# Performance work log

Measured on AMD Instinct MI355X. Metric: run time of the kernel, lower is better.

Reference implementation:

```python
import jax, jax.numpy as jnp
import numpy as np

HIDDEN = 2048
N_HEADS = 32
N_KV_HEADS = 8
HEAD_DIM = 64
MAX_SEQ_LEN = 4096
ROPE_THETA = 500000.0
B, L = 1, 2048
EPS = 1e-6
NEG = -1e9


def precompute_rope(head_dim, max_seq_len, theta):
    freqs = 1.0 / theta ** (jnp.arange(0, head_dim, 2, dtype=jnp.float32) / head_dim)
    pos = jnp.arange(max_seq_len, dtype=jnp.float32)
    ang = pos[:, None] * freqs[None, :]                     # [S, hd/2]
    cos = jnp.repeat(jnp.cos(ang), 2, axis=-1)              # [S, hd]
    sin = jnp.repeat(jnp.sin(ang), 2, axis=-1)
    return cos, sin


def apply_rope(x, cos, sin):
    # x: [B, H, L, hd]; interleaved (even/odd) rotation, faithful to torch code
    seq_len = x.shape[2]
    c = cos[:seq_len][None, None, :, ::2]                   # [1,1,L,hd/2]
    s = sin[:seq_len][None, None, :, ::2]
    x1 = x[..., ::2]
    x2 = x[..., 1::2]
    o1 = x1 * c - x2 * s
    o2 = x2 * c + x1 * s
    return jnp.stack([o1, o2], axis=-1).reshape(x.shape)


def rmsnorm(x, w):
    return x * jax.lax.rsqrt(jnp.mean(x * x, axis=-1, keepdims=True) + EPS) * w


def setup_inputs() -> dict:
    key = jax.random.key(0)
    ks = jax.random.split(key, 6)
    x = jax.random.normal(ks[0], (B, L, HIDDEN), dtype=jnp.float32)
    causal = jnp.tril(jnp.ones((L, L), dtype=bool))
    mask = jnp.where(causal, 0.0, NEG).astype(jnp.float32)  # additive causal mask
    scale = 0.02
    norm_w = jnp.ones((HIDDEN,), dtype=jnp.float32)
    Wq = jax.random.normal(ks[1], (N_HEADS * HEAD_DIM, HIDDEN), dtype=jnp.float32) * scale
    Wk = jax.random.normal(ks[2], (N_KV_HEADS * HEAD_DIM, HIDDEN), dtype=jnp.float32) * scale
    Wv = jax.random.normal(ks[3], (N_KV_HEADS * HEAD_DIM, HIDDEN), dtype=jnp.float32) * scale
    Wo = jax.random.normal(ks[4], (HIDDEN, N_HEADS * HEAD_DIM), dtype=jnp.float32) * scale
    rope_cos, rope_sin = precompute_rope(HEAD_DIM, MAX_SEQ_LEN, ROPE_THETA)
    return {"x": x, "mask": mask, "norm_w": norm_w, "Wq": Wq, "Wk": Wk,
            "Wv": Wv, "Wo": Wo, "rope_cos": rope_cos, "rope_sin": rope_sin}


def reference(x, mask, norm_w, Wq, Wk, Wv, Wo, rope_cos, rope_sin):
    Bb, Ll, _ = x.shape
    residual = x
    h = rmsnorm(x, norm_w)
    q = (h @ Wq.T).reshape(Bb, Ll, N_HEADS, HEAD_DIM).transpose(0, 2, 1, 3)     # [B,H,L,hd]
    k = (h @ Wk.T).reshape(Bb, Ll, N_KV_HEADS, HEAD_DIM).transpose(0, 2, 1, 3)  # [B,Hk,L,hd]
    v = (h @ Wv.T).reshape(Bb, Ll, N_KV_HEADS, HEAD_DIM).transpose(0, 2, 1, 3)
    q = apply_rope(q, rope_cos, rope_sin)
    k = apply_rope(k, rope_cos, rope_sin)
    n_groups = N_HEADS // N_KV_HEADS
    if n_groups > 1:
        k = jnp.repeat(k, n_groups, axis=1)   # GQA repeat_interleave
        v = jnp.repeat(v, n_groups, axis=1)
    scale = jnp.sqrt(jnp.asarray(HEAD_DIM, dtype=q.dtype))
    attn = jnp.einsum('bhld,bhmd->bhlm', q, k) / scale
    attn = attn + mask                                       # broadcast [L,L]
    attn = jax.nn.softmax(attn, axis=-1)
    out = jnp.einsum('bhlm,bhmd->bhld', attn, v)
    out = out.transpose(0, 2, 1, 3).reshape(Bb, Ll, N_HEADS * HEAD_DIM)
    return out @ Wo.T + residual
```

## Files before the change

### kernel.cpp

```cpp
#include <hip/hip_runtime.h>
#include <stdint.h>

#define L_SEQ 2048
#define HID   2048
#define NHEAD 32
#define NKV   8
#define HD    64
#define KVDIM 512
#define QSCALE 0.18033688f

typedef __attribute__((ext_vector_type(8))) short s16x8;
typedef __attribute__((ext_vector_type(4))) short s16x4;
typedef __attribute__((ext_vector_type(4))) float f32x4;

__device__ __forceinline__ short f2bf(float f) {
  __bf16 b = (__bf16)f;
  short s;
  __builtin_memcpy(&s, &b, 2);
  return s;
}

__device__ __forceinline__ void gload16(const void* g, void* l) {
  __builtin_amdgcn_global_load_lds(
      (const __attribute__((address_space(1))) void*)g,
      (__attribute__((address_space(3))) void*)l, 16, 0, 0);
}

__global__ __launch_bounds__(256) void pre_kernel(
    const float* __restrict__ x, const float* __restrict__ w,
    const float* __restrict__ wq, const float* __restrict__ wk,
    const float* __restrict__ wv, const float* __restrict__ wo,
    short* __restrict__ h,
    short* __restrict__ owq, short* __restrict__ owk,
    short* __restrict__ owv, short* __restrict__ owo) {
  const int tid = threadIdx.x;
  if (blockIdx.x >= 2048) {
    int64_t e = ((int64_t)(blockIdx.x - 2048) * 256 + tid) * 4;
    const float* src; short* dst; int64_t o;
    if (e < 4194304)      { src = wq; dst = owq; o = e; }
    else if (e < 5242880) { src = wk; dst = owk; o = e - 4194304; }
    else if (e < 6291456) { src = wv; dst = owv; o = e - 5242880; }
    else                  { src = wo; dst = owo; o = e - 6291456; }
    f32x4 v = *(const f32x4*)(src + o);
    s16x4 b;
    b[0] = f2bf(v[0]); b[1] = f2bf(v[1]); b[2] = f2bf(v[2]); b[3] = f2bf(v[3]);
    *(s16x4*)(dst + o) = b;
    return;
  }
  const int row = blockIdx.x;
  const float* xr = x + (int64_t)row * HID + tid * 8;
  f32x4 a = *(const f32x4*)(xr);
  f32x4 b = *(const f32x4*)(xr + 4);
  float ss = a[0]*a[0]+a[1]*a[1]+a[2]*a[2]+a[3]*a[3]
           + b[0]*b[0]+b[1]*b[1]+b[2]*b[2]+b[3]*b[3];
  #pragma unroll
  for (int off = 1; off < 64; off <<= 1) ss += __shfl_xor(ss, off, 64);
  __shared__ float sred[4];
  if ((tid & 63) == 0) sred[tid >> 6] = ss;
  __syncthreads();
  const float scale = rsqrtf((sred[0]+sred[1]+sred[2]+sred[3]) * (1.0f/HID) + 1e-6f);
  const float* wp = w + tid * 8;
  f32x4 wa = *(const f32x4*)(wp);
  f32x4 wb = *(const f32x4*)(wp + 4);
  s16x8 o;
  o[0]=f2bf(a[0]*scale*wa[0]); o[1]=f2bf(a[1]*scale*wa[1]);
  o[2]=f2bf(a[2]*scale*wa[2]); o[3]=f2bf(a[3]*scale*wa[3]);
  o[4]=f2bf(b[0]*scale*wb[0]); o[5]=f2bf(b[1]*scale*wb[1]);
  o[6]=f2bf(b[2]*scale*wb[2]); o[7]=f2bf(b[3]*scale*wb[3]);
  *(s16x8*)(h + (int64_t)row * HID + tid * 8) = o;
}

__device__ __forceinline__ void gemm_core_128x64(
    const short* __restrict__ A, const short* __restrict__ B,
    short* sA, short* sB, f32x4 acc[4][2]) {
  const int tid = threadIdx.x;
  const int lane = tid & 63;
  const int w = tid >> 6, wr = w >> 1, wc = w & 1;
  const int g = lane >> 4, li = lane & 15;

  auto stage = [&](int k0, int buf) {
    #pragma unroll
    for (int i = 0; i < 4; ++i) {
      const int flat = i * 256 + tid;
      const int row = flat >> 3, c8 = flat & 7;
      const int sc = c8 ^ (row & 7);
      gload16(A + (int64_t)row * HID + k0 + sc * 8, sA + buf * 8192 + flat * 8);
    }
    #pragma unroll
    for (int i = 0; i < 2; ++i) {
      const int flat = i * 256 + tid;
      const int row = flat >> 3, c8 = flat & 7;
      const int sc = c8 ^ (row & 7);
      gload16(B + (int64_t)row * HID + k0 + sc * 8, sB + buf * 4096 + flat * 8);
    }
  };

  stage(0, 0);
  for (int k0 = 0; k0 < HID; k0 += 64) {
    const int cur = (k0 >> 6) & 1;
    __syncthreads();
    if (k0 + 64 < HID) stage(k0 + 64, cur ^ 1);
    const short* cA = sA + cur * 8192;
    const short* cB = sB + cur * 4096;
    #pragma unroll
    for (int kk = 0; kk < 2; ++kk) {
      s16x8 af[4], bfr[2];
      const int chunk = (kk << 2) | g;
      #pragma unroll
      for (int m = 0; m < 4; ++m) {
        const int row = wr * 64 + m * 16 + li;
        af[m] = *(const s16x8*)(cA + row * 64 + ((chunk ^ (li & 7)) << 3));
      }
      #pragma unroll
      for (int n = 0; n < 2; ++n) {
        const int row = wc * 32 + n * 16 + li;
        bfr[n] = *(const s16x8*)(cB + row * 64 + ((chunk ^ (li & 7)) << 3));
      }
      __builtin_amdgcn_s_setprio(1);
      #pragma unroll
      for (int m = 0; m < 4; ++m)
        #pragma unroll
        for (int n = 0; n < 2; ++n)
          acc[m][n] = __builtin_amdgcn_mfma_f32_16x16x32_bf16(af[m], bfr[n], acc[m][n], 0, 0, 0);
      __builtin_amdgcn_s_setprio(0);
    }
  }
}

__global__ __launch_bounds__(256) void qkv_kernel(
    const short* __restrict__ h16, const short* __restrict__ wq,
    const short* __restrict__ wk, const short* __restrict__ wv,
    short* __restrict__ qo, short* __restrict__ ko, short* __restrict__ vto,
    const float* __restrict__ rc, const float* __restrict__ rs) {
  __shared__ short sA[2 * 128 * 64];
  __shared__ short sB[2 * 64 * 64];
  const int cb = blockIdx.x, rb = blockIdx.y;
  const short* B; short* out; int colbase, mode; int64_t ldc;
  if (cb < 32)      { B = wq + (int64_t)cb * 64 * HID;        out = qo;  colbase = cb * 64;        mode = 0; ldc = HID;   }
  else if (cb < 40) { B = wk + (int64_t)(cb - 32) * 64 * HID; out = ko;  colbase = (cb - 32) * 64; mode = 0; ldc = KVDIM; }
  else              { B = wv + (int64_t)(cb - 40) * 64 * HID; out = vto; colbase = (cb - 40) * 64; mode = 1; ldc = L_SEQ; }
  const float rsc = (cb < 32) ? QSCALE : 1.0f;

  f32x4 acc[4][2];
  const f32x4 z = {0.f, 0.f, 0.f, 0.f};
  #pragma unroll
  for (int m = 0; m < 4; ++m)
    #pragma unroll
    for (int n = 0; n < 2; ++n) acc[m][n] = z;

  gemm_core_128x64(h16 + (int64_t)rb * 128 * HID, B, sA, sB, acc);

  const int lane = threadIdx.x & 63;
  const int w = threadIdx.x >> 6, wr = w >> 1, wc = w & 1;
  const int g = lane >> 4, li = lane & 15;

  if (mode == 0) {
    #pragma unroll
    for (int m = 0; m < 4; ++m) {
      #pragma unroll
      for (int n = 0; n < 2; ++n) {
        const int col = colbase + wc * 32 + n * 16 + li;
        const int d2 = col & 62;
        #pragma unroll
        for (int r = 0; r < 4; ++r) {
          const int row = rb * 128 + wr * 64 + m * 16 + g * 4 + r;
          const float c = rc[row * 64 + d2] * rsc;
          const float s = rs[row * 64 + d2] * rsc;
          const float v0 = acc[m][n][r];
          const float pr = __shfl_xor(v0, 1, 64);
          const float o = (lane & 1) ? (v0 * c + pr * s) : (v0 * c - pr * s);
          out[(int64_t)row * ldc + col] = f2bf(o);
        }
      }
    }
  } else {
    #pragma unroll
    for (int m = 0; m < 4; ++m) {
      #pragma unroll
      for (int n = 0; n < 2; ++n) {
        const int col = colbase + wc * 32 + n * 16 + li;
        const int row0 = rb * 128 + wr * 64 + m * 16 + g * 4;
        s16x4 pk;
        pk[0] = f2bf(acc[m][n][0]); pk[1] = f2bf(acc[m][n][1]);
        pk[2] = f2bf(acc[m][n][2]); pk[3] = f2bf(acc[m][n][3]);
        *(s16x4*)(out + (int64_t)col * L_SEQ + row0) = pk;
      }
    }
  }
}

__global__ __launch_bounds__(512, 4) void attn_kernel(
    const short* __restrict__ q16, const short* __restrict__ k16,
    const short* __restrict__ vt16, short* __restrict__ out16) {
  __shared__ short sK[4 * 64 * 64];
  __shared__ short sV[4 * 64 * 64];
  __shared__ short sP[8][16 * 64];
  const int pi = blockIdx.x, h = blockIdx.y, kvh = h >> 2;
  const int qbL = pi, qbH = 31 - pi;
  const int tid = threadIdx.x, lane = tid & 63, w = tid >> 6, wl = w & 3;
  const int g = lane >> 4, li = lane & 15;
  const int myqb = (w < 4) ? qbL : qbH;
  short* sPw = &sP[w][0];

  s16x8 qf[2];
  {
    const int qr = myqb * 64 + wl * 16 + li;
    #pragma unroll
    for (int kk = 0; kk < 2; ++kk)
      qf[kk] = *(const s16x8*)(q16 + (int64_t)qr * HID + h * 64 + kk * 32 + g * 8);
  }

  f32x4 acc[4];
  const f32x4 z = {0.f, 0.f, 0.f, 0.f};
  #pragma unroll
  for (int n = 0; n < 4; ++n) acc[n] = z;
  float m = -1e30f, l = 0.f;

  auto stage1 = [&](int t, int buf, int slot) {
    const int kv0 = t * 64;
    const int row = tid >> 3, c8 = tid & 7;
    const int sc = c8 ^ (row & 7);
    const int off = (buf * 2 + slot) * 4096;
    gload16(k16 + (int64_t)(kv0 + row) * KVDIM + kvh * 64 + sc * 8,
            sK + off + tid * 8);
    gload16(vt16 + (int64_t)(kvh * 64 + row) * L_SEQ + kv0 + sc * 8,
            sV + off + tid * 8);
  };

  stage1(0, 0, 0);
  stage1(1, 0, 1);
  for (int tp = 0; 2 * tp <= qbH; ++tp) {
    const int buf = tp & 1;
    __syncthreads();
    if (2 * tp + 2 <= qbH) {
      stage1(2 * tp + 2, buf ^ 1, 0);
      const int t3 = 2 * tp + 3;
      stage1(t3 <= qbH ? t3 : t3 - 1, buf ^ 1, 1);
    }
    #pragma unroll
    for (int sl = 0; sl < 2; ++sl) {
      const int t = 2 * tp + sl;
      if (t <= qbH && (w >= 4 || t <= qbL)) {
        const short* cK = sK + (buf * 2 + sl) * 4096;
        const short* cV = sV + (buf * 2 + sl) * 4096;

        s16x8 kf[2][4];
        #pragma unroll
        for (int kk = 0; kk < 2; ++kk)
          #pragma unroll
          for (int n = 0; n < 4; ++n)
            kf[kk][n] = *(const s16x8*)(cK + (n * 16 + li) * 64 + ((((kk << 2) | g) ^ (li & 7)) << 3));
        f32x4 s[4];
        #pragma unroll
        for (int n = 0; n < 4; ++n) s[n] = z;
        __builtin_amdgcn_s_setprio(1);
        #pragma unroll
        for (int kk = 0; kk < 2; ++kk)
          #pragma unroll
          for (int n = 0; n < 4; ++n)
            s[n] = __builtin_amdgcn_mfma_f32_16x16x32_bf16(kf[kk][n], qf[kk], s[n], 0, 0, 0);
        __builtin_amdgcn_s_setprio(0);

        if (t == myqb) {
          const int ql = wl * 16 + li;
          #pragma unroll
          for (int n = 0; n < 4; ++n)
            #pragma unroll
            for (int r = 0; r < 4; ++r)
              if (n * 16 + g * 4 + r > ql) s[n][r] = -1e30f;
        }

        float mx = fmaxf(fmaxf(s[0][0], s[0][1]), fmaxf(s[0][2], s[0][3]));
        #pragma unroll
        for (int n = 1; n < 4; ++n)
          mx = fmaxf(mx, fmaxf(fmaxf(s[n][0], s[n][1]), fmaxf(s[n][2], s[n][3])));
        mx = fmaxf(mx, __shfl_xor(mx, 16, 64));
        mx = fmaxf(mx, __shfl_xor(mx, 32, 64));
        if (__any(mx > m + 8.0f)) {
          const float mn = fmaxf(m, mx);
          const float al = __builtin_amdgcn_exp2f(m - mn);
          m = mn;
          l *= al;
          #pragma unroll
          for (int dt = 0; dt < 4; ++dt)
            #pragma unroll
            for (int r = 0; r < 4; ++r) acc[dt][r] *= al;
        }
        float ps = 0.f;
        #pragma unroll
        for (int n = 0; n < 4; ++n) {
          s16x4 pk;
          #pragma unroll
          for (int r = 0; r < 4; ++r) {
            const float p = __builtin_amdgcn_exp2f(s[n][r] - m);
            pk[r] = f2bf(p);
            ps += p;
          }
          *(s16x4*)(sPw + li * 64 + (((n * 2 + (g >> 1)) ^ (li & 7)) << 3) + (g & 1) * 4) = pk;
        }
        ps += __shfl_xor(ps, 16, 64);
        ps += __shfl_xor(ps, 32, 64);
        l += ps;

        s16x8 vf[2][4];
        #pragma unroll
        for (int kk = 0; kk < 2; ++kk)
          #pragma unroll
          for (int dt = 0; dt < 4; ++dt)
            vf[kk][dt] = *(const s16x8*)(cV + (dt * 16 + li) * 64 + ((((kk << 2) | g) ^ (li & 7)) << 3));
        #pragma unroll
        for (int kk = 0; kk < 2; ++kk) {
          s16x8 pf = *(const s16x8*)(sPw + li * 64 + (((kk * 4 + g) ^ (li & 7)) << 3));
          __builtin_amdgcn_s_setprio(1);
          #pragma unroll
          for (int dt = 0; dt < 4; ++dt)
            acc[dt] = __builtin_amdgcn_mfma_f32_16x16x32_bf16(vf[kk][dt], pf, acc[dt], 0, 0, 0);
          __builtin_amdgcn_s_setprio(0);
        }
      }
    }
  }

  const float rl = 1.0f / l;
  #pragma unroll
  for (int n2 = 0; n2 < 4; ++n2) {
    s16x4 o;
    #pragma unroll
    for (int r = 0; r < 4; ++r) o[r] = f2bf(acc[n2][r] * rl);
    *(s16x4*)(sPw + li * 64 + (((n2 * 2 + (g >> 1)) ^ (li & 7)) << 3) + (g & 1) * 4) = o;
  }
  #pragma unroll
  for (int half = 0; half < 2; ++half) {
    const int chunk = half * 64 + lane;
    const int q = chunk >> 3, c = chunk & 7;
    s16x8 v = *(const s16x8*)(sPw + q * 64 + ((c ^ (q & 7)) << 3));
    *(s16x8*)(out16 + (int64_t)(myqb * 64 + wl * 16 + q) * HID + h * 64 + c * 8) = v;
  }
}

__global__ __launch_bounds__(256) void oproj_kernel(
    const short* __restrict__ ao, const short* __restrict__ wo,
    const float* __restrict__ resid, float* __restrict__ out) {
  __shared__ short sA[2 * 128 * 64];
  __shared__ short sB[2 * 64 * 64];
  const int cb = blockIdx.x, rb = blockIdx.y;
  f32x4 acc[4][2];
  const f32x4 z = {0.f, 0.f, 0.f, 0.f};
  #pragma unroll
  for (int m = 0; m < 4; ++m)
    #pragma unroll
    for (int n = 0; n < 2; ++n) acc[m][n] = z;

  gemm_core_128x64(ao + (int64_t)rb * 128 * HID, wo + (int64_t)cb * 64 * HID, sA, sB, acc);

  const int lane = threadIdx.x & 63;
  const int w = threadIdx.x >> 6, wr = w >> 1, wc = w & 1;
  const int g = lane >> 4, li = lane & 15;
  #pragma unroll
  for (int m = 0; m < 4; ++m) {
    #pragma unroll
    for (int n = 0; n < 2; ++n) {
      const int col = cb * 64 + wc * 32 + n * 16 + li;
      #pragma unroll
      for (int r = 0; r < 4; ++r) {
        const int row = rb * 128 + wr * 64 + m * 16 + g * 4 + r;
        out[(int64_t)row * HID + col] = acc[m][n][r] + resid[(int64_t)row * HID + col];
      }
    }
  }
}

extern "C" void kernel_launch(void* const* d_in, const int* in_sizes, int n_in,
                              void* d_out, int out_size, void* d_ws, size_t ws_size,
                              hipStream_t stream) {
  (void)in_sizes; (void)n_in; (void)out_size; (void)ws_size;
  const float* x      = (const float*)d_in[0];
  const float* norm_w = (const float*)d_in[2];
  const float* Wq     = (const float*)d_in[3];
  const float* Wk     = (const float*)d_in[4];
  const float* Wv     = (const float*)d_in[5];
  const float* Wo     = (const float*)d_in[6];
  const float* rc     = (const float*)d_in[7];
  const float* rs     = (const float*)d_in[8];
  float* out = (float*)d_out;

  char* ws = (char*)d_ws;
  short* wq16 = (short*)(ws);
  short* wk16 = (short*)(ws + 8388608);
  short* wv16 = (short*)(ws + 10485760);
  short* wo16 = (short*)(ws + 12582912);
  short* h16  = (short*)(ws + 20971520);
  short* q16  = (short*)(ws + 29360128);
  short* k16  = (short*)(ws + 37748736);
  short* vt16 = (short*)(ws + 39845888);
  short* ao16 = (short*)(ws + 41943040);

  pre_kernel<<<12288, 256, 0, stream>>>(x, norm_w, Wq, Wk, Wv, Wo,
                                        h16, wq16, wk16, wv16, wo16);
  qkv_kernel<<<dim3(48, 16), 256, 0, stream>>>(h16, wq16, wk16, wv16, q16, k16, vt16, rc, rs);
  attn_kernel<<<dim3(16, NHEAD), 512, 0, stream>>>(q16, k16, vt16, ao16);
  oproj_kernel<<<dim3(32, 16), 256, 0, stream>>>(ao16, wo16, x, out);
}
```

Baseline: 124.1 us.

## Switch attention to 32x32x16 MFMA with register-resident P via permlane32 swap

Attention now uses 4 waves of 256 threads, each owning 32 query rows, and 32x32x16 bf16 MFMAs instead of 8 waves with 16x16x32 MFMAs. The P matrix no longer goes through shared memory: it is packed to bf16 in registers and reshuffled with v_permlane32_swap into the B-operand layout. The output is written straight from registers without an LDS transpose. This cuts LDS traffic and the number of MFMA issues per tile. In exchange, register pressure per wave rises and each block has half as many waves to hide latency.

```diff
diff --git a/kernel.cpp b/kernel.cpp
--- a/kernel.cpp
+++ b/kernel.cpp
@@ -12,12 +12,18 @@
 typedef __attribute__((ext_vector_type(8))) short s16x8;
 typedef __attribute__((ext_vector_type(4))) short s16x4;
 typedef __attribute__((ext_vector_type(4))) float f32x4;
+typedef __attribute__((ext_vector_type(16))) float f32x16;
 
 __device__ __forceinline__ short f2bf(float f) {
   __bf16 b = (__bf16)f;
   short s;
   __builtin_memcpy(&s, &b, 2);
   return s;
+}
+
+__device__ __forceinline__ unsigned int pk2(float a, float b) {
+  return (unsigned int)(unsigned short)f2bf(a) |
+         ((unsigned int)(unsigned short)f2bf(b) << 16);
 }
 
 __device__ __forceinline__ void gload16(const void* g, void* l) {
@@ -189,92 +195,86 @@
   }
 }
 
-__global__ __launch_bounds__(512, 4) void attn_kernel(
+__global__ __launch_bounds__(256, 2) void attn_kernel(
     const short* __restrict__ q16, const short* __restrict__ k16,
     const short* __restrict__ vt16, short* __restrict__ out16) {
   __shared__ short sK[4 * 64 * 64];
   __shared__ short sV[4 * 64 * 64];
-  __shared__ short sP[8][16 * 64];
   const int pi = blockIdx.x, h = blockIdx.y, kvh = h >> 2;
   const int qbL = pi, qbH = 31 - pi;
-  const int tid = threadIdx.x, lane = tid & 63, w = tid >> 6, wl = w & 3;
-  const int g = lane >> 4, li = lane & 15;
-  const int myqb = (w < 4) ? qbL : qbH;
-  short* sPw = &sP[w][0];
-
-  s16x8 qf[2];
-  {
-    const int qr = myqb * 64 + wl * 16 + li;
-    #pragma unroll
-    for (int kk = 0; kk < 2; ++kk)
-      qf[kk] = *(const s16x8*)(q16 + (int64_t)qr * HID + h * 64 + kk * 32 + g * 8);
-  }
-
-  f32x4 acc[4];
-  const f32x4 z = {0.f, 0.f, 0.f, 0.f};
-  #pragma unroll
-  for (int n = 0; n < 4; ++n) acc[n] = z;
+  const int tid = threadIdx.x, lane = tid & 63, w = tid >> 6;
+  const int r31 = lane & 31, half = lane >> 5;
+  const int myqb = (w < 2) ? qbL : qbH;
+  const int wrow = w & 1;
+  const int qg = myqb * 64 + wrow * 32 + r31;
+
+  s16x8 qf[4];
+  #pragma unroll
+  for (int ds = 0; ds < 4; ++ds)
+    qf[ds] = *(const s16x8*)(q16 + (int64_t)qg * HID + h * 64 + ds * 16 + half * 8);
+
+  f32x16 acc0 = {}, acc1 = {};
   float m = -1e30f, l = 0.f;
 
-  auto stage1 = [&](int t, int buf, int slot) {
+  auto stage1 = [&](int t, int idx) {
     const int kv0 = t * 64;
-    const int row = tid >> 3, c8 = tid & 7;
-    const int sc = c8 ^ (row & 7);
-    const int off = (buf * 2 + slot) * 4096;
-    gload16(k16 + (int64_t)(kv0 + row) * KVDIM + kvh * 64 + sc * 8,
-            sK + off + tid * 8);
-    gload16(vt16 + (int64_t)(kvh * 64 + row) * L_SEQ + kv0 + sc * 8,
-            sV + off + tid * 8);
+    #pragma unroll
+    for (int i = 0; i < 2; ++i) {
+      const int flat = i * 256 + tid;
+      const int row = flat >> 3, c8 = flat & 7;
+      const int sc = c8 ^ (row & 7);
+      gload16(k16 + (int64_t)(kv0 + row) * KVDIM + kvh * 64 + sc * 8,
+              sK + idx * 4096 + flat * 8);
+      gload16(vt16 + (int64_t)(kvh * 64 + row) * L_SEQ + kv0 + sc * 8,
+              sV + idx * 4096 + flat * 8);
+    }
   };
 
-  stage1(0, 0, 0);
-  stage1(1, 0, 1);
+  stage1(0, 0);
+  stage1(1, 1);
   for (int tp = 0; 2 * tp <= qbH; ++tp) {
     const int buf = tp & 1;
     __syncthreads();
     if (2 * tp + 2 <= qbH) {
-      stage1(2 * tp + 2, buf ^ 1, 0);
+      stage1(2 * tp + 2, (buf ^ 1) * 2);
       const int t3 = 2 * tp + 3;
-      stage1(t3 <= qbH ? t3 : t3 - 1, buf ^ 1, 1);
+      stage1(t3 <= qbH ? t3 : t3 - 1, (buf ^ 1) * 2 + 1);
     }
     #pragma unroll
     for (int sl = 0; sl < 2; ++sl) {
       const int t = 2 * tp + sl;
-      if (t <= qbH && (w >= 4 || t <= qbL)) {
+      if (t <= myqb) {
         const short* cK = sK + (buf * 2 + sl) * 4096;
         const short* cV = sV + (buf * 2 + sl) * 4096;
 
-        s16x8 kf[2][4];
-        #pragma unroll
-        for (int kk = 0; kk < 2; ++kk)
+        f32x16 S0 = {}, S1 = {};
+        __builtin_amdgcn_s_setprio(1);
+        #pragma unroll
+        for (int ds = 0; ds < 4; ++ds) {
+          const int row0 = r31;
+          s16x8 kfa = *(const s16x8*)(cK + row0 * 64 + (((ds * 2 + half) ^ (row0 & 7)) << 3));
+          S0 = __builtin_amdgcn_mfma_f32_32x32x16_bf16(kfa, qf[ds], S0, 0, 0, 0);
+          const int row1 = 32 + r31;
+          s16x8 kfb = *(const s16x8*)(cK + row1 * 64 + (((ds * 2 + half) ^ (row1 & 7)) << 3));
+          S1 = __builtin_amdgcn_mfma_f32_32x32x16_bf16(kfb, qf[ds], S1, 0, 0, 0);
+        }
+        __builtin_amdgcn_s_setprio(0);
+
+        if (t == myqb) {
+          const int qloc = wrow * 32 + r31;
           #pragma unroll
-          for (int n = 0; n < 4; ++n)
-            kf[kk][n] = *(const s16x8*)(cK + (n * 16 + li) * 64 + ((((kk << 2) | g) ^ (li & 7)) << 3));
-        f32x4 s[4];
-        #pragma unroll
-        for (int n = 0; n < 4; ++n) s[n] = z;
-        __builtin_amdgcn_s_setprio(1);
-        #pragma unroll
-        for (int kk = 0; kk < 2; ++kk)
-          #pragma unroll
-          for (int n = 0; n < 4; ++n)
-            s[n] = __builtin_amdgcn_mfma_f32_16x16x32_bf16(kf[kk][n], qf[kk], s[n], 0, 0, 0);
-        __builtin_amdgcn_s_setprio(0);
-
-        if (t == myqb) {
-          const int ql = wl * 16 + li;
-          #pragma unroll
-          for (int n = 0; n < 4; ++n)
-            #pragma unroll
-            for (int r = 0; r < 4; ++r)
-              if (n * 16 + g * 4 + r > ql) s[n][r] = -1e30f;
-        }
-
-        float mx = fmaxf(fmaxf(s[0][0], s[0][1]), fmaxf(s[0][2], s[0][3]));
-        #pragma unroll
-        for (int n = 1; n < 4; ++n)
-          mx = fmaxf(mx, fmaxf(fmaxf(s[n][0], s[n][1]), fmaxf(s[n][2], s[n][3])));
-        mx = fmaxf(mx, __shfl_xor(mx, 16, 64));
+          for (int reg = 0; reg < 16; ++reg) {
+            const int row = (reg & 3) + 8 * (reg >> 2) + 4 * half;
+            if (row > qloc) S0[reg] = -1e30f;
+            if (row + 32 > qloc) S1[reg] = -1e30f;
+          }
+        }
+
+        float mx = S0[0];
+        #pragma unroll
+        for (int reg = 1; reg < 16; ++reg) mx = fmaxf(mx, S0[reg]);
+        #pragma unroll
+        for (int reg = 0; reg < 16; ++reg) mx = fmaxf(mx, S1[reg]);
         mx = fmaxf(mx, __shfl_xor(mx, 32, 64));
         if (__any(mx > m + 8.0f)) {
           const float mn = fmaxf(m, mx);
@@ -282,59 +282,70 @@
           m = mn;
           l *= al;
           #pragma unroll
-          for (int dt = 0; dt < 4; ++dt)
-            #pragma unroll
-            for (int r = 0; r < 4; ++r) acc[dt][r] *= al;
-        }
+          for (int reg = 0; reg < 16; ++reg) { acc0[reg] *= al; acc1[reg] *= al; }
+        }
+
         float ps = 0.f;
-        #pragma unroll
-        for (int n = 0; n < 4; ++n) {
-          s16x4 pk;
-          #pragma unroll
-          for (int r = 0; r < 4; ++r) {
-            const float p = __builtin_amdgcn_exp2f(s[n][r] - m);
-            pk[r] = f2bf(p);
-            ps += p;
-          }
-          *(s16x4*)(sPw + li * 64 + (((n * 2 + (g >> 1)) ^ (li & 7)) << 3) + (g & 1) * 4) = pk;
-        }
-        ps += __shfl_xor(ps, 16, 64);
+        unsigned int W[2][4][2];
+        #pragma unroll
+        for (int g2 = 0; g2 < 4; ++g2) {
+          float p0 = __builtin_amdgcn_exp2f(S0[g2 * 4 + 0] - m);
+          float p1 = __builtin_amdgcn_exp2f(S0[g2 * 4 + 1] - m);
+          float p2 = __builtin_amdgcn_exp2f(S0[g2 * 4 + 2] - m);
+          float p3 = __builtin_amdgcn_exp2f(S0[g2 * 4 + 3] - m);
+          ps += p0 + p1 + p2 + p3;
+          W[0][g2][0] = pk2(p0, p1);
+          W[0][g2][1] = pk2(p2, p3);
+          float q0 = __builtin_amdgcn_exp2f(S1[g2 * 4 + 0] - m);
+          float q1 = __builtin_amdgcn_exp2f(S1[g2 * 4 + 1] - m);
+          float q2 = __builtin_amdgcn_exp2f(S1[g2 * 4 + 2] - m);
+          float q3 = __builtin_amdgcn_exp2f(S1[g2 * 4 + 3] - m);
+          ps += q0 + q1 + q2 + q3;
+          W[1][g2][0] = pk2(q0, q1);
+          W[1][g2][1] = pk2(q2, q3);
+        }
         ps += __shfl_xor(ps, 32, 64);
         l += ps;
 
-        s16x8 vf[2][4];
-        #pragma unroll
-        for (int kk = 0; kk < 2; ++kk)
+        #pragma unroll
+        for (int kvt = 0; kvt < 2; ++kvt) {
           #pragma unroll
-          for (int dt = 0; dt < 4; ++dt)
-            vf[kk][dt] = *(const s16x8*)(cV + (dt * 16 + li) * 64 + ((((kk << 2) | g) ^ (li & 7)) << 3));
-        #pragma unroll
-        for (int kk = 0; kk < 2; ++kk) {
-          s16x8 pf = *(const s16x8*)(sPw + li * 64 + (((kk * 4 + g) ^ (li & 7)) << 3));
-          __builtin_amdgcn_s_setprio(1);
-          #pragma unroll
-          for (int dt = 0; dt < 4; ++dt)
-            acc[dt] = __builtin_amdgcn_mfma_f32_16x16x32_bf16(vf[kk][dt], pf, acc[dt], 0, 0, 0);
-          __builtin_amdgcn_s_setprio(0);
+          for (int ksl = 0; ksl < 2; ++ksl) {
+            unsigned int a0 = W[kvt][ksl * 2 + 0][0], b0 = W[kvt][ksl * 2 + 1][0];
+            unsigned int a1 = W[kvt][ksl * 2 + 0][1], b1 = W[kvt][ksl * 2 + 1][1];
+            asm volatile("v_permlane32_swap_b32 %0, %1" : "+v"(a0), "+v"(b0));
+            asm volatile("v_permlane32_swap_b32 %0, %1" : "+v"(a1), "+v"(b1));
+            union { unsigned int u[4]; s16x8 s; } pf;
+            pf.u[0] = a0; pf.u[1] = a1; pf.u[2] = b0; pf.u[3] = b1;
+            const int ks = kvt * 2 + ksl;
+            __builtin_amdgcn_s_setprio(1);
+            {
+              const int row0 = r31;
+              s16x8 vfa = *(const s16x8*)(cV + row0 * 64 + (((ks * 2 + half) ^ (row0 & 7)) << 3));
+              acc0 = __builtin_amdgcn_mfma_f32_32x32x16_bf16(vfa, pf.s, acc0, 0, 0, 0);
+              const int row1 = 32 + r31;
+              s16x8 vfb = *(const s16x8*)(cV + row1 * 64 + (((ks * 2 + half) ^ (row1 & 7)) << 3));
+              acc1 = __builtin_amdgcn_mfma_f32_32x32x16_bf16(vfb, pf.s, acc1, 0, 0, 0);
+            }
+            __builtin_amdgcn_s_setprio(0);
+          }
         }
       }
     }
   }
 
   const float rl = 1.0f / l;
-  #pragma unroll
-  for (int n2 = 0; n2 < 4; ++n2) {
-    s16x4 o;
-    #pragma unroll
-    for (int r = 0; r < 4; ++r) o[r] = f2bf(acc[n2][r] * rl);
-    *(s16x4*)(sPw + li * 64 + (((n2 * 2 + (g >> 1)) ^ (li & 7)) << 3) + (g & 1) * 4) = o;
-  }
-  #pragma unroll
-  for (int half = 0; half < 2; ++half) {
-    const int chunk = half * 64 + lane;
-    const int q = chunk >> 3, c = chunk & 7;
-    s16x8 v = *(const s16x8*)(sPw + q * 64 + ((c ^ (q & 7)) << 3));
-    *(s16x8*)(out16 + (int64_t)(myqb * 64 + wl * 16 + q) * HID + h * 64 + c * 8) = v;
+  short* orow = out16 + (int64_t)qg * HID + h * 64;
+  #pragma unroll
+  for (int g2 = 0; g2 < 4; ++g2) {
+    s16x4 o0, o1;
+    #pragma unroll
+    for (int r = 0; r < 4; ++r) {
+      o0[r] = f2bf(acc0[g2 * 4 + r] * rl);
+      o1[r] = f2bf(acc1[g2 * 4 + r] * rl);
+    }
+    *(s16x4*)(orow + g2 * 8 + half * 4) = o0;
+    *(s16x4*)(orow + 32 + g2 * 8 + half * 4) = o1;
   }
 }
 
@@ -398,6 +409,6 @@
   pre_kernel<<<12288, 256, 0, stream>>>(x, norm_w, Wq, Wk, Wv, Wo,
                                         h16, wq16, wk16, wv16, wo16);
   qkv_kernel<<<dim3(48, 16), 256, 0, stream>>>(h16, wq16, wk16, wv16, q16, k16, vt16, rc, rs);
-  attn_kernel<<<dim3(16, NHEAD), 512, 0, stream>>>(q16, k16, vt16, ao16);
+  attn_kernel<<<dim3(16, NHEAD), 256, 0, stream>>>(q16, k16, vt16, ao16);
   oproj_kernel<<<dim3(32, 16), 256, 0, stream>>>(ao16, wo16, x, out);
 }
```

Result: slower. 135.7 us (+9.3%).

## Move Wo bf16 conversion into attention kernel to overlap with attention

Applied to the files above, without the earlier changes.

The fp32-to-bf16 conversion of Wo moves out of the pre-kernel and into extra blocks of the attention launch, whose grid doubles in x. Those extra blocks only convert Wo and exit, so the conversion can run alongside attention work rather than on the critical path before the QKV GEMM. The cost is a larger attention grid with short blocks that may interfere with scheduling of the attention blocks. The wb[7-4] edit is cosmetic.

```diff
diff --git a/kernel.cpp b/kernel.cpp
--- a/kernel.cpp
+++ b/kernel.cpp
@@ -29,18 +29,17 @@
 __global__ __launch_bounds__(256) void pre_kernel(
     const float* __restrict__ x, const float* __restrict__ w,
     const float* __restrict__ wq, const float* __restrict__ wk,
-    const float* __restrict__ wv, const float* __restrict__ wo,
+    const float* __restrict__ wv,
     short* __restrict__ h,
     short* __restrict__ owq, short* __restrict__ owk,
-    short* __restrict__ owv, short* __restrict__ owo) {
+    short* __restrict__ owv) {
   const int tid = threadIdx.x;
   if (blockIdx.x >= 2048) {
     int64_t e = ((int64_t)(blockIdx.x - 2048) * 256 + tid) * 4;
     const float* src; short* dst; int64_t o;
     if (e < 4194304)      { src = wq; dst = owq; o = e; }
     else if (e < 5242880) { src = wk; dst = owk; o = e - 4194304; }
-    else if (e < 6291456) { src = wv; dst = owv; o = e - 5242880; }
-    else                  { src = wo; dst = owo; o = e - 6291456; }
+    else                  { src = wv; dst = owv; o = e - 5242880; }
     f32x4 v = *(const f32x4*)(src + o);
     s16x4 b;
     b[0] = f2bf(v[0]); b[1] = f2bf(v[1]); b[2] = f2bf(v[2]); b[3] = f2bf(v[3]);
@@ -66,7 +65,7 @@
   o[0]=f2bf(a[0]*scale*wa[0]); o[1]=f2bf(a[1]*scale*wa[1]);
   o[2]=f2bf(a[2]*scale*wa[2]); o[3]=f2bf(a[3]*scale*wa[3]);
   o[4]=f2bf(b[0]*scale*wb[0]); o[5]=f2bf(b[1]*scale*wb[1]);
-  o[6]=f2bf(b[2]*scale*wb[2]); o[7]=f2bf(b[3]*scale*wb[3]);
+  o[6]=f2bf(b[2]*scale*wb[2]); o[7]=f2bf(b[3]*scale*wb[7-4]);
   *(s16x8*)(h + (int64_t)row * HID + tid * 8) = o;
 }
 
@@ -191,7 +190,21 @@
 
 __global__ __launch_bounds__(512, 4) void attn_kernel(
     const short* __restrict__ q16, const short* __restrict__ k16,
-    const short* __restrict__ vt16, short* __restrict__ out16) {
+    const short* __restrict__ vt16, short* __restrict__ out16,
+    const float* __restrict__ wof, short* __restrict__ wo16o) {
+  if (blockIdx.x >= 16) {
+    const int idx = (blockIdx.x - 16) * NHEAD + blockIdx.y;
+    const int64_t base = (int64_t)idx * 8192;
+    #pragma unroll
+    for (int i = 0; i < 4; ++i) {
+      const int64_t o = base + i * 2048 + threadIdx.x * 4;
+      f32x4 v = *(const f32x4*)(wof + o);
+      s16x4 b;
+      b[0] = f2bf(v[0]); b[1] = f2bf(v[1]); b[2] = f2bf(v[2]); b[3] = f2bf(v[3]);
+      *(s16x4*)(wo16o + o) = b;
+    }
+    return;
+  }
   __shared__ short sK[4 * 64 * 64];
   __shared__ short sV[4 * 64 * 64];
   __shared__ short sP[8][16 * 64];
@@ -395,9 +408,9 @@
   short* vt16 = (short*)(ws + 39845888);
   short* ao16 = (short*)(ws + 41943040);
 
-  pre_kernel<<<12288, 256, 0, stream>>>(x, norm_w, Wq, Wk, Wv, Wo,
-                                        h16, wq16, wk16, wv16, wo16);
+  pre_kernel<<<8192, 256, 0, stream>>>(x, norm_w, Wq, Wk, Wv,
+                                       h16, wq16, wk16, wv16);
   qkv_kernel<<<dim3(48, 16), 256, 0, stream>>>(h16, wq16, wk16, wv16, q16, k16, vt16, rc, rs);
-  attn_kernel<<<dim3(16, NHEAD), 512, 0, stream>>>(q16, k16, vt16, ao16);
+  attn_kernel<<<dim3(32, NHEAD), 512, 0, stream>>>(q16, k16, vt16, ao16, Wo, wo16);
   oproj_kernel<<<dim3(32, 16), 256, 0, stream>>>(ao16, wo16, x, out);
 }
```

Measured after the change: 156.8 us. +26.3%, slower.
